# Performance work log

Hardware: AMD Instinct MI355X
Metric: run time of the kernel (lower is better)

## Reference

```python
import jax, jax.numpy as jnp
import numpy as np

N_NODES = 50000
N_EDGES = 600000
N_GRAPHS = 128
D = 128
L = 3
OUT = 10
BN_EPS = 1e-5


def setup_inputs() -> dict:
    key = jax.random.key(0)
    ks = jax.random.split(key, 8)
    x = jax.random.normal(ks[0], (N_NODES, D), dtype=jnp.float32)
    edge_index = jax.random.randint(ks[1], (2, N_EDGES), 0, N_NODES, dtype=jnp.int64)
    batch = jnp.sort(jax.random.randint(ks[2], (N_NODES,), 0, N_GRAPHS, dtype=jnp.int64))
    s = 0.05
    return {
        "x": x,
        "edge_index": edge_index,
        "batch": batch,
        "convW1": jax.random.normal(ks[3], (L, D, D), dtype=jnp.float32) * s,
        "convb1": jnp.zeros((L, D), dtype=jnp.float32),
        "convg": jnp.ones((L, D), dtype=jnp.float32),
        "convbt": jnp.zeros((L, D), dtype=jnp.float32),
        "convW2": jax.random.normal(ks[4], (L, D, D), dtype=jnp.float32) * s,
        "convb2": jnp.zeros((L, D), dtype=jnp.float32),
        "mW1": jax.random.normal(ks[5], (D, D), dtype=jnp.float32) * s,
        "mb1": jnp.zeros((D,), dtype=jnp.float32),
        "mg": jnp.ones((D,), dtype=jnp.float32),
        "mbt": jnp.zeros((D,), dtype=jnp.float32),
        "mW2": jax.random.normal(ks[6], (D, OUT), dtype=jnp.float32) * s,
        "mb2": jnp.zeros((OUT,), dtype=jnp.float32),
    }


def _mlp(h, W1, b1, g, bt, W2, b2):
    # PyG MLP: Linear -> BatchNorm(eval: mean=0, var=1) -> ReLU -> Linear (plain last)
    inv = 1.0 / jnp.sqrt(1.0 + BN_EPS)
    h = h @ W1 + b1
    h = jnp.maximum(h * (inv * g) + bt, 0.0)
    return h @ W2 + b2


def reference(x, edge_index, batch, convW1, convb1, convg, convbt, convW2, convb2,
              mW1, mb1, mg, mbt, mW2, mb2):
    src, dst = edge_index[0], edge_index[1]
    for l in range(L):
        # GINConv (eps=0): nn(x + scatter-add of neighbor features)
        agg = jax.ops.segment_sum(x[src], dst, num_segments=N_NODES)  # [N, D]
        x = _mlp(x + agg, convW1[l], convb1[l], convg[l], convbt[l], convW2[l], convb2[l])
        x = jnp.maximum(x, 0.0)  # .relu() after conv
    pooled = jax.ops.segment_sum(x, batch, num_segments=N_GRAPHS)  # [G, D]
    return _mlp(pooled, mW1, mb1, mg, mbt, mW2, mb2)  # [G, OUT]
```

## Files before the change

### kernel.cpp

```cpp
#include <hip/hip_runtime.h>

#define N_NODES 50000
#define N_EDGES 600000
#define N_GRAPHS 128
#define DIM 128
#define NLAYERS 3
#define NOUT 10
#define ELLW 48
#define LSTRIDE 136
#define ZROW N_NODES

typedef unsigned short u16;
typedef __attribute__((ext_vector_type(8))) short bf16x8;
typedef __attribute__((ext_vector_type(4))) float f32x4;

__device__ __forceinline__ float bf2f(u16 v) {
    unsigned u = ((unsigned)v) << 16;
    return __builtin_bit_cast(float, u);
}
__device__ __forceinline__ u16 f2bf(float f) {
    unsigned u = __builtin_bit_cast(unsigned, f);
    u = u + 0x7fffu + ((u >> 16) & 1u);
    return (u16)(u >> 16);
}

__global__ void zero_small(int* __restrict__ deg, float* __restrict__ pooled) {
    int i = blockIdx.x * blockDim.x + threadIdx.x;
    if (i < N_NODES) deg[i] = 0;
    if (i < N_GRAPHS * DIM) pooled[i] = 0.f;
}

__global__ void prep_all(int* __restrict__ deg, u16* __restrict__ ell,
                         const int* __restrict__ srcs, const int* __restrict__ dsts,
                         u16* __restrict__ xb, u16* __restrict__ bufA, u16* __restrict__ bufB,
                         const float* __restrict__ x, u16* __restrict__ Wswz,
                         const float* __restrict__ convW1, const float* __restrict__ convW2) {
    int i = blockIdx.x * blockDim.x + threadIdx.x;
    if (i < N_EDGES) {
        int d = dsts[i];
        int slot = atomicAdd(&deg[d], 1);
        if (slot < ELLW) ell[(size_t)d * ELLW + slot] = (u16)srcs[i];
    }
    if (i < DIM) {
        xb[(size_t)ZROW * DIM + i] = 0;
        bufA[(size_t)ZROW * DIM + i] = 0;
        bufB[(size_t)ZROW * DIM + i] = 0;
    }
    if (i < 6 * 16384) {
        int j = i & 7, lane = (i >> 3) & 63, cb = (i >> 9) & 7, kc = (i >> 12) & 3, w = i >> 14;
        int k = kc * 32 + ((lane >> 4) << 3) + j;
        int c = (cb << 4) + (lane & 15);
        const float* W = (w < 3) ? (convW1 + (size_t)w * 16384) : (convW2 + (size_t)(w - 3) * 16384);
        Wswz[i] = f2bf(W[k * DIM + c]);
    }
    if (i < N_NODES * DIM / 4) {
        float4 v = ((const float4*)x)[i];
        ushort4 o;
        o.x = f2bf(v.x); o.y = f2bf(v.y); o.z = f2bf(v.z); o.w = f2bf(v.w);
        ((ushort4*)xb)[i] = o;
    }
}

template <int POOL>
__global__ __launch_bounds__(256) void layer_fused(
    u16* __restrict__ out, const u16* __restrict__ x,
    const int* __restrict__ deg, const u16* __restrict__ ell,
    const u16* __restrict__ W1f, const u16* __restrict__ W2f,
    const float* __restrict__ b1, const float* __restrict__ g1,
    const float* __restrict__ bt1, const float* __restrict__ b2,
    const int* __restrict__ batch, float* __restrict__ pooled) {
    __shared__ u16 A[16 * LSTRIDE];
    __shared__ u16 H[16 * LSTRIDE];
    __shared__ int gb[16];
    const int tid = threadIdx.x;
    const int wv = tid >> 6;
    const int lane = tid & 63;
    const int row0 = blockIdx.x * 16;

    if (POOL && tid < 16) gb[tid] = batch[row0 + tid];

    const size_t coff = (size_t)lane * 2;
    {
        const int r0 = wv << 2;
        int len[4];
        const u16* ep[4];
        float ax[4], ay[4];
#pragma unroll
        for (int r = 0; r < 4; ++r) {
            const int grow = row0 + r0 + r;
            len[r] = min(deg[grow], ELLW);
            ep[r] = ell + (size_t)grow * ELLW;
            ushort2 self = *(const ushort2*)(x + (size_t)grow * DIM + coff);
            ax[r] = bf2f(self.x);
            ay[r] = bf2f(self.y);
        }
        const int maxlen = max(max(len[0], len[1]), max(len[2], len[3]));
        for (int j = 0; j < maxlen; j += 4) {
            int id[4][4];
#pragma unroll
            for (int r = 0; r < 4; ++r) {
                ushort4 e = *(const ushort4*)(ep[r] + j);
                id[r][0] = (j + 0 < len[r]) ? (int)e.x : ZROW;
                id[r][1] = (j + 1 < len[r]) ? (int)e.y : ZROW;
                id[r][2] = (j + 2 < len[r]) ? (int)e.z : ZROW;
                id[r][3] = (j + 3 < len[r]) ? (int)e.w : ZROW;
            }
#pragma unroll
            for (int r = 0; r < 4; ++r) {
                float px = 0.f, py = 0.f;
#pragma unroll
                for (int t = 0; t < 4; ++t) {
                    ushort2 v = *(const ushort2*)(x + (size_t)id[r][t] * DIM + coff);
                    px += bf2f(v.x);
                    py += bf2f(v.y);
                }
                ax[r] += px;
                ay[r] += py;
            }
        }
#pragma unroll
        for (int r = 0; r < 4; ++r) {
            ushort2 o;
            o.x = f2bf(ax[r]);
            o.y = f2bf(ay[r]);
            *(ushort2*)&A[(r0 + r) * LSTRIDE + lane * 2] = o;
        }
    }
    __syncthreads();

    const float inv = rsqrtf(1.f + 1e-5f);
    const int col0 = lane & 15;
    const int rbl = (lane >> 4) << 2;
    const int fragoff = (lane & 15) * LSTRIDE + ((lane >> 4) << 3);

    {
        f32x4 acc[2];
        acc[0] = (f32x4){0.f, 0.f, 0.f, 0.f};
        acc[1] = (f32x4){0.f, 0.f, 0.f, 0.f};
#pragma unroll
        for (int kc = 0; kc < 4; ++kc) {
            bf16x8 a = *(const bf16x8*)&A[fragoff + kc * 32];
#pragma unroll
            for (int m = 0; m < 2; ++m) {
                const int cb = (wv << 1) + m;
                bf16x8 bb = *(const bf16x8*)(W1f + ((((kc << 3) + cb) << 6 | lane) << 3));
                acc[m] = __builtin_amdgcn_mfma_f32_16x16x32_bf16(a, bb, acc[m], 0, 0, 0);
            }
        }
#pragma unroll
        for (int m = 0; m < 2; ++m) {
            const int c = (((wv << 1) + m) << 4) + col0;
            const float bias = b1[c];
            const float sg = inv * g1[c];
            const float st = bt1[c];
#pragma unroll
            for (int q = 0; q < 4; ++q) {
                float v = (acc[m][q] + bias) * sg + st;
                H[(rbl + q) * LSTRIDE + c] = f2bf(fmaxf(v, 0.f));
            }
        }
    }
    __syncthreads();

    {
        f32x4 acc[2];
        acc[0] = (f32x4){0.f, 0.f, 0.f, 0.f};
        acc[1] = (f32x4){0.f, 0.f, 0.f, 0.f};
#pragma unroll
        for (int kc = 0; kc < 4; ++kc) {
            bf16x8 a = *(const bf16x8*)&H[fragoff + kc * 32];
#pragma unroll
            for (int m = 0; m < 2; ++m) {
                const int cb = (wv << 1) + m;
                bf16x8 bb = *(const bf16x8*)(W2f + ((((kc << 3) + cb) << 6 | lane) << 3));
                acc[m] = __builtin_amdgcn_mfma_f32_16x16x32_bf16(a, bb, acc[m], 0, 0, 0);
            }
        }
#pragma unroll
        for (int m = 0; m < 2; ++m) {
            const int c = (((wv << 1) + m) << 4) + col0;
            const float bias = b2[c];
#pragma unroll
            for (int q = 0; q < 4; ++q) {
                float v = acc[m][q] + bias;
                A[(rbl + q) * LSTRIDE + c] = f2bf(fmaxf(v, 0.f));
            }
        }
    }
    __syncthreads();

    if (!POOL) {
        const int r = tid >> 4;
        const int seg = tid & 15;
        uint4 v = *(const uint4*)&A[r * LSTRIDE + seg * 8];
        *(uint4*)(out + (size_t)(row0 + r) * DIM + seg * 8) = v;
    } else {
        const int c = tid & 127;
        const int rbeg = (tid >> 7) << 3;
        float acc = 0.f;
        int curg = gb[rbeg];
#pragma unroll
        for (int r = 0; r < 8; ++r) {
            const int g = gb[rbeg + r];
            if (g != curg) {
                atomicAdd(&pooled[(size_t)curg * DIM + c], acc);
                acc = 0.f;
                curg = g;
            }
            acc += bf2f(A[(rbeg + r) * LSTRIDE + c]);
        }
        atomicAdd(&pooled[(size_t)curg * DIM + c], acc);
    }
}

__global__ __launch_bounds__(128) void tail_mlp(float* __restrict__ out,
                                                const float* __restrict__ pooled,
                                                const float* __restrict__ mW1,
                                                const float* __restrict__ mb1,
                                                const float* __restrict__ mg,
                                                const float* __restrict__ mbt,
                                                const float* __restrict__ mW2,
                                                const float* __restrict__ mb2) {
    const int g = blockIdx.x;
    const int c = threadIdx.x;
    __shared__ float pl[DIM];
    __shared__ float hd[DIM];
    pl[c] = pooled[(size_t)g * DIM + c];
    __syncthreads();

    float s = 0.f;
#pragma unroll 4
    for (int k = 0; k < DIM; ++k) s += pl[k] * mW1[k * DIM + c];
    const float inv = rsqrtf(1.f + 1e-5f);
    s = (s + mb1[c]) * (inv * mg[c]) + mbt[c];
    hd[c] = fmaxf(s, 0.f);
    __syncthreads();

    if (c < NOUT) {
        float o = 0.f;
#pragma unroll 4
        for (int k = 0; k < DIM; ++k) o += hd[k] * mW2[k * NOUT + c];
        out[g * NOUT + c] = o + mb2[c];
    }
}

extern "C" void kernel_launch(void* const* d_in, const int* in_sizes, int n_in,
                              void* d_out, int out_size, void* d_ws, size_t ws_size,
                              hipStream_t stream) {
    const float* x      = (const float*)d_in[0];
    const int*   ei     = (const int*)d_in[1];
    const int*   batch  = (const int*)d_in[2];
    const float* convW1 = (const float*)d_in[3];
    const float* convb1 = (const float*)d_in[4];
    const float* convg  = (const float*)d_in[5];
    const float* convbt = (const float*)d_in[6];
    const float* convW2 = (const float*)d_in[7];
    const float* convb2 = (const float*)d_in[8];
    const float* mW1    = (const float*)d_in[9];
    const float* mb1    = (const float*)d_in[10];
    const float* mg     = (const float*)d_in[11];
    const float* mbt    = (const float*)d_in[12];
    const float* mW2    = (const float*)d_in[13];
    const float* mb2    = (const float*)d_in[14];
    float* out = (float*)d_out;

    const int* srcs = ei;
    const int* dsts = ei + N_EDGES;

    const size_t NFP = (size_t)(N_NODES + 1) * DIM;
    u16* xb0  = (u16*)d_ws;
    u16* bufA = xb0 + NFP;
    u16* bufB = bufA + NFP;
    u16* Wswz = bufB + NFP;
    float* pooled = (float*)(Wswz + 6 * 16384);
    int* deg = (int*)(pooled + N_GRAPHS * DIM);
    u16* ell = (u16*)(deg + N_NODES);

    zero_small<<<(N_NODES + 255) / 256, 256, 0, stream>>>(deg, pooled);
    prep_all<<<(N_NODES * DIM / 4 + 255) / 256, 256, 0, stream>>>(
        deg, ell, srcs, dsts, xb0, bufA, bufB, x, Wswz, convW1, convW2);

    const int layerBlocks = N_NODES / 16;
    layer_fused<0><<<layerBlocks, 256, 0, stream>>>(
        bufA, xb0, deg, ell, Wswz, Wswz + (size_t)3 * 16384,
        convb1, convg, convbt, convb2, batch, pooled);
    layer_fused<0><<<layerBlocks, 256, 0, stream>>>(
        bufB, bufA, deg, ell, Wswz + (size_t)1 * 16384, Wswz + (size_t)4 * 16384,
        convb1 + DIM, convg + DIM, convbt + DIM, convb2 + DIM, batch, pooled);
    layer_fused<1><<<layerBlocks, 256, 0, stream>>>(
        bufA , bufB, deg, ell, Wswz + (size_t)2 * 16384, Wswz + (size_t)5 * 16384,
        convb1 + 2 * DIM, convg + 2 * DIM, convbt + 2 * DIM, convb2 + 2 * DIM, batch, pooled);

    tail_mlp<<<N_GRAPHS, 128, 0, stream>>>(out, pooled, mW1, mb1, mg, mbt, mW2, mb2);
}
```

Before: 154.8 us.

## Build ELL adjacency via two-pass bucketing with shared-memory per-bucket assembly

Replaces per-node global atomics and scattered 2-byte ELL writes with a two-phase build. Edges are first binned into 128-node buckets using one global atomic per edge on 391 counters. A new kernel then assembles each bucket's ELL rows in shared memory and writes them out with coalesced 16-byte stores. This adds a kernel launch and an intermediate buffer, and raises contention on the bucket counters. Edges beyond the bucket capacity of 2048 are silently dropped, which is only safe while the average is around 1536 per bucket.

```diff
diff --git a/kernel.cpp b/kernel.cpp
--- a/kernel.cpp
+++ b/kernel.cpp
@@ -9,8 +9,11 @@
 #define ELLW 48
 #define LSTRIDE 136
 #define ZROW N_NODES
+#define NBKT 391
+#define BKT_CAP 2048
 
 typedef unsigned short u16;
+typedef unsigned int u32;
 typedef __attribute__((ext_vector_type(8))) short bf16x8;
 typedef __attribute__((ext_vector_type(4))) float f32x4;
 
@@ -24,13 +27,13 @@
     return (u16)(u >> 16);
 }
 
-__global__ void zero_small(int* __restrict__ deg, float* __restrict__ pooled) {
+__global__ void zero_small(int* __restrict__ bcnt, float* __restrict__ pooled) {
     int i = blockIdx.x * blockDim.x + threadIdx.x;
-    if (i < N_NODES) deg[i] = 0;
+    if (i < NBKT) bcnt[i] = 0;
     if (i < N_GRAPHS * DIM) pooled[i] = 0.f;
 }
 
-__global__ void prep_all(int* __restrict__ deg, u16* __restrict__ ell,
+__global__ void prep_all(int* __restrict__ bcnt, u32* __restrict__ bpairs,
                          const int* __restrict__ srcs, const int* __restrict__ dsts,
                          u16* __restrict__ xb, u16* __restrict__ bufA, u16* __restrict__ bufB,
                          const float* __restrict__ x, u16* __restrict__ Wswz,
@@ -38,8 +41,10 @@
     int i = blockIdx.x * blockDim.x + threadIdx.x;
     if (i < N_EDGES) {
         int d = dsts[i];
-        int slot = atomicAdd(&deg[d], 1);
-        if (slot < ELLW) ell[(size_t)d * ELLW + slot] = (u16)srcs[i];
+        int b = d >> 7;
+        int pos = atomicAdd(&bcnt[b], 1);
+        if (pos < BKT_CAP)
+            bpairs[(size_t)b * BKT_CAP + pos] = ((u32)srcs[i] << 16) | (u32)(d & 127);
     }
     if (i < DIM) {
         xb[(size_t)ZROW * DIM + i] = 0;
@@ -58,6 +63,36 @@
         ushort4 o;
         o.x = f2bf(v.x); o.y = f2bf(v.y); o.z = f2bf(v.z); o.w = f2bf(v.w);
         ((ushort4*)xb)[i] = o;
+    }
+}
+
+__global__ __launch_bounds__(256) void ell_build(u16* __restrict__ ell, int* __restrict__ deg,
+                                                 const u32* __restrict__ bpairs,
+                                                 const int* __restrict__ bcnt) {
+    __shared__ u16 ell_s[128 * ELLW];
+    __shared__ int deg_s[128];
+    const int b = blockIdx.x;
+    const int tid = threadIdx.x;
+    if (tid < 128) deg_s[tid] = 0;
+    __syncthreads();
+
+    const int cnt = min(bcnt[b], BKT_CAP);
+    const u32* bp = bpairs + (size_t)b * BKT_CAP;
+    for (int i = tid; i < cnt; i += 256) {
+        u32 p = bp[i];
+        int local = (int)(p & 0xFFFFu);
+        int slot = atomicAdd(&deg_s[local], 1);
+        if (slot < ELLW) ell_s[local * ELLW + slot] = (u16)(p >> 16);
+    }
+    __syncthreads();
+
+    const int node0 = b << 7;
+    if (tid < 128 && node0 + tid < N_NODES) deg[node0 + tid] = deg_s[tid];
+    u16* eout = ell + (size_t)node0 * ELLW;
+#pragma unroll
+    for (int t = 0; t < 3; ++t) {
+        const int i = tid + t * 256;
+        *(uint4*)(eout + i * 8) = *(const uint4*)(ell_s + i * 8);
     }
 }
 
@@ -273,12 +308,15 @@
     u16* bufB = bufA + NFP;
     u16* Wswz = bufB + NFP;
     float* pooled = (float*)(Wswz + 6 * 16384);
-    int* deg = (int*)(pooled + N_GRAPHS * DIM);
-    u16* ell = (u16*)(deg + N_NODES);
-
-    zero_small<<<(N_NODES + 255) / 256, 256, 0, stream>>>(deg, pooled);
+    int* bcnt = (int*)(pooled + N_GRAPHS * DIM);
+    int* deg  = bcnt + 512;
+    u32* bpairs = (u32*)(deg + N_NODES);
+    u16* ell = (u16*)(bpairs + (size_t)NBKT * BKT_CAP);
+
+    zero_small<<<(N_GRAPHS * DIM + 255) / 256, 256, 0, stream>>>(bcnt, pooled);
     prep_all<<<(N_NODES * DIM / 4 + 255) / 256, 256, 0, stream>>>(
-        deg, ell, srcs, dsts, xb0, bufA, bufB, x, Wswz, convW1, convW2);
+        bcnt, bpairs, srcs, dsts, xb0, bufA, bufB, x, Wswz, convW1, convW2);
+    ell_build<<<NBKT, 256, 0, stream>>>(ell, deg, bpairs, bcnt);
 
     const int layerBlocks = N_NODES / 16;
     layer_fused<0><<<layerBlocks, 256, 0, stream>>>(
```

Result: slower. 336.9 us (+117.6%).

## Process 32 rows per block in fused GIN layer and split prep kernel

Applied to the files above, without the earlier changes.

Doubles the row tile of the fused layer kernel from 16 to 32 rows, so each wave gathers 8 rows and issues two MFMA row tiles per weight fragment load. This halves the per-row cost of loading weights and reduces the block count, but raises register pressure and the gather loop now runs to the maximum degree over 8 rows. Out-of-range rows are clamped to the zero row and their stores are masked. The prep kernel is also split into separate edge-to-ELL and conversion kernels.

```diff
diff --git a/kernel.cpp b/kernel.cpp
--- a/kernel.cpp
+++ b/kernel.cpp
@@ -9,8 +9,10 @@
 #define ELLW 48
 #define LSTRIDE 136
 #define ZROW N_NODES
+#define TROWS 32
 
 typedef unsigned short u16;
+typedef unsigned int u32;
 typedef __attribute__((ext_vector_type(8))) short bf16x8;
 typedef __attribute__((ext_vector_type(4))) float f32x4;
 
@@ -26,21 +28,23 @@
 
 __global__ void zero_small(int* __restrict__ deg, float* __restrict__ pooled) {
     int i = blockIdx.x * blockDim.x + threadIdx.x;
-    if (i < N_NODES) deg[i] = 0;
+    if (i < N_NODES + 16) deg[i] = 0;
     if (i < N_GRAPHS * DIM) pooled[i] = 0.f;
 }
 
-__global__ void prep_all(int* __restrict__ deg, u16* __restrict__ ell,
-                         const int* __restrict__ srcs, const int* __restrict__ dsts,
-                         u16* __restrict__ xb, u16* __restrict__ bufA, u16* __restrict__ bufB,
+__global__ void prep_ell(int* __restrict__ deg, u16* __restrict__ ell,
+                         const int* __restrict__ srcs, const int* __restrict__ dsts) {
+    int i = blockIdx.x * blockDim.x + threadIdx.x;
+    if (i >= N_EDGES) return;
+    int d = dsts[i];
+    int slot = atomicAdd(&deg[d], 1);
+    if (slot < ELLW) ell[(size_t)d * ELLW + slot] = (u16)srcs[i];
+}
+
+__global__ void prep_cvt(u16* __restrict__ xb, u16* __restrict__ bufA, u16* __restrict__ bufB,
                          const float* __restrict__ x, u16* __restrict__ Wswz,
                          const float* __restrict__ convW1, const float* __restrict__ convW2) {
     int i = blockIdx.x * blockDim.x + threadIdx.x;
-    if (i < N_EDGES) {
-        int d = dsts[i];
-        int slot = atomicAdd(&deg[d], 1);
-        if (slot < ELLW) ell[(size_t)d * ELLW + slot] = (u16)srcs[i];
-    }
     if (i < DIM) {
         xb[(size_t)ZROW * DIM + i] = 0;
         bufA[(size_t)ZROW * DIM + i] = 0;
@@ -69,36 +73,38 @@
     const float* __restrict__ b1, const float* __restrict__ g1,
     const float* __restrict__ bt1, const float* __restrict__ b2,
     const int* __restrict__ batch, float* __restrict__ pooled) {
-    __shared__ u16 A[16 * LSTRIDE];
-    __shared__ u16 H[16 * LSTRIDE];
-    __shared__ int gb[16];
+    __shared__ u16 A[TROWS * LSTRIDE];
+    __shared__ u16 H[TROWS * LSTRIDE];
+    __shared__ int gb[TROWS];
     const int tid = threadIdx.x;
     const int wv = tid >> 6;
     const int lane = tid & 63;
-    const int row0 = blockIdx.x * 16;
-
-    if (POOL && tid < 16) gb[tid] = batch[row0 + tid];
+    const int row0 = blockIdx.x * TROWS;
+
+    if (POOL && tid < TROWS) gb[tid] = batch[min(row0 + tid, N_NODES - 1)];
 
     const size_t coff = (size_t)lane * 2;
     {
-        const int r0 = wv << 2;
-        int len[4];
-        const u16* ep[4];
-        float ax[4], ay[4];
-#pragma unroll
-        for (int r = 0; r < 4; ++r) {
-            const int grow = row0 + r0 + r;
+        const int r0 = wv << 3;
+        int len[8];
+        const u16* ep[8];
+        float ax[8], ay[8];
+#pragma unroll
+        for (int r = 0; r < 8; ++r) {
+            const int grow = min(row0 + r0 + r, ZROW);
             len[r] = min(deg[grow], ELLW);
             ep[r] = ell + (size_t)grow * ELLW;
             ushort2 self = *(const ushort2*)(x + (size_t)grow * DIM + coff);
             ax[r] = bf2f(self.x);
             ay[r] = bf2f(self.y);
         }
-        const int maxlen = max(max(len[0], len[1]), max(len[2], len[3]));
+        int maxlen = 0;
+#pragma unroll
+        for (int r = 0; r < 8; ++r) maxlen = max(maxlen, len[r]);
         for (int j = 0; j < maxlen; j += 4) {
-            int id[4][4];
-#pragma unroll
-            for (int r = 0; r < 4; ++r) {
+            int id[8][4];
+#pragma unroll
+            for (int r = 0; r < 8; ++r) {
                 ushort4 e = *(const ushort4*)(ep[r] + j);
                 id[r][0] = (j + 0 < len[r]) ? (int)e.x : ZROW;
                 id[r][1] = (j + 1 < len[r]) ? (int)e.y : ZROW;
@@ -106,7 +112,7 @@
                 id[r][3] = (j + 3 < len[r]) ? (int)e.w : ZROW;
             }
 #pragma unroll
-            for (int r = 0; r < 4; ++r) {
+            for (int r = 0; r < 8; ++r) {
                 float px = 0.f, py = 0.f;
 #pragma unroll
                 for (int t = 0; t < 4; ++t) {
@@ -119,7 +125,7 @@
             }
         }
 #pragma unroll
-        for (int r = 0; r < 4; ++r) {
+        for (int r = 0; r < 8; ++r) {
             ushort2 o;
             o.x = f2bf(ax[r]);
             o.y = f2bf(ay[r]);
@@ -131,20 +137,25 @@
     const float inv = rsqrtf(1.f + 1e-5f);
     const int col0 = lane & 15;
     const int rbl = (lane >> 4) << 2;
-    const int fragoff = (lane & 15) * LSTRIDE + ((lane >> 4) << 3);
+    const int fo0 = (lane & 15) * LSTRIDE + ((lane >> 4) << 3);
+    const int fo1 = (16 + (lane & 15)) * LSTRIDE + ((lane >> 4) << 3);
 
     {
-        f32x4 acc[2];
-        acc[0] = (f32x4){0.f, 0.f, 0.f, 0.f};
-        acc[1] = (f32x4){0.f, 0.f, 0.f, 0.f};
+        f32x4 acc[2][2];
+#pragma unroll
+        for (int rt = 0; rt < 2; ++rt)
+#pragma unroll
+            for (int m = 0; m < 2; ++m) acc[rt][m] = (f32x4){0.f, 0.f, 0.f, 0.f};
 #pragma unroll
         for (int kc = 0; kc < 4; ++kc) {
-            bf16x8 a = *(const bf16x8*)&A[fragoff + kc * 32];
+            bf16x8 a0 = *(const bf16x8*)&A[fo0 + kc * 32];
+            bf16x8 a1 = *(const bf16x8*)&A[fo1 + kc * 32];
 #pragma unroll
             for (int m = 0; m < 2; ++m) {
                 const int cb = (wv << 1) + m;
                 bf16x8 bb = *(const bf16x8*)(W1f + ((((kc << 3) + cb) << 6 | lane) << 3));
-                acc[m] = __builtin_amdgcn_mfma_f32_16x16x32_bf16(a, bb, acc[m], 0, 0, 0);
+                acc[0][m] = __builtin_amdgcn_mfma_f32_16x16x32_bf16(a0, bb, acc[0][m], 0, 0, 0);
+                acc[1][m] = __builtin_amdgcn_mfma_f32_16x16x32_bf16(a1, bb, acc[1][m], 0, 0, 0);
             }
         }
 #pragma unroll
@@ -154,26 +165,33 @@
             const float sg = inv * g1[c];
             const float st = bt1[c];
 #pragma unroll
-            for (int q = 0; q < 4; ++q) {
-                float v = (acc[m][q] + bias) * sg + st;
-                H[(rbl + q) * LSTRIDE + c] = f2bf(fmaxf(v, 0.f));
+            for (int rt = 0; rt < 2; ++rt) {
+#pragma unroll
+                for (int q = 0; q < 4; ++q) {
+                    float v = (acc[rt][m][q] + bias) * sg + st;
+                    H[(rt * 16 + rbl + q) * LSTRIDE + c] = f2bf(fmaxf(v, 0.f));
+                }
             }
         }
     }
     __syncthreads();
 
     {
-        f32x4 acc[2];
-        acc[0] = (f32x4){0.f, 0.f, 0.f, 0.f};
-        acc[1] = (f32x4){0.f, 0.f, 0.f, 0.f};
+        f32x4 acc[2][2];
+#pragma unroll
+        for (int rt = 0; rt < 2; ++rt)
+#pragma unroll
+            for (int m = 0; m < 2; ++m) acc[rt][m] = (f32x4){0.f, 0.f, 0.f, 0.f};
 #pragma unroll
         for (int kc = 0; kc < 4; ++kc) {
-            bf16x8 a = *(const bf16x8*)&H[fragoff + kc * 32];
+            bf16x8 a0 = *(const bf16x8*)&H[fo0 + kc * 32];
+            bf16x8 a1 = *(const bf16x8*)&H[fo1 + kc * 32];
 #pragma unroll
             for (int m = 0; m < 2; ++m) {
                 const int cb = (wv << 1) + m;
                 bf16x8 bb = *(const bf16x8*)(W2f + ((((kc << 3) + cb) << 6 | lane) << 3));
-                acc[m] = __builtin_amdgcn_mfma_f32_16x16x32_bf16(a, bb, acc[m], 0, 0, 0);
+                acc[0][m] = __builtin_amdgcn_mfma_f32_16x16x32_bf16(a0, bb, acc[0][m], 0, 0, 0);
+                acc[1][m] = __builtin_amdgcn_mfma_f32_16x16x32_bf16(a1, bb, acc[1][m], 0, 0, 0);
             }
         }
 #pragma unroll
@@ -181,26 +199,33 @@
             const int c = (((wv << 1) + m) << 4) + col0;
             const float bias = b2[c];
 #pragma unroll
-            for (int q = 0; q < 4; ++q) {
-                float v = acc[m][q] + bias;
-                A[(rbl + q) * LSTRIDE + c] = f2bf(fmaxf(v, 0.f));
+            for (int rt = 0; rt < 2; ++rt) {
+#pragma unroll
+                for (int q = 0; q < 4; ++q) {
+                    float v = acc[rt][m][q] + bias;
+                    A[(rt * 16 + rbl + q) * LSTRIDE + c] = f2bf(fmaxf(v, 0.f));
+                }
             }
         }
     }
     __syncthreads();
 
     if (!POOL) {
-        const int r = tid >> 4;
-        const int seg = tid & 15;
-        uint4 v = *(const uint4*)&A[r * LSTRIDE + seg * 8];
-        *(uint4*)(out + (size_t)(row0 + r) * DIM + seg * 8) = v;
+#pragma unroll
+        for (int it = 0; it < 2; ++it) {
+            const int r = (tid >> 4) + it * 16;
+            const int seg = tid & 15;
+            const int grow = row0 + r;
+            uint4 v = *(const uint4*)&A[r * LSTRIDE + seg * 8];
+            if (grow < N_NODES) *(uint4*)(out + (size_t)grow * DIM + seg * 8) = v;
+        }
     } else {
         const int c = tid & 127;
-        const int rbeg = (tid >> 7) << 3;
+        const int rbeg = (tid >> 7) << 4;
         float acc = 0.f;
         int curg = gb[rbeg];
 #pragma unroll
-        for (int r = 0; r < 8; ++r) {
+        for (int r = 0; r < 16; ++r) {
             const int g = gb[rbeg + r];
             if (g != curg) {
                 atomicAdd(&pooled[(size_t)curg * DIM + c], acc);
@@ -274,13 +299,14 @@
     u16* Wswz = bufB + NFP;
     float* pooled = (float*)(Wswz + 6 * 16384);
     int* deg = (int*)(pooled + N_GRAPHS * DIM);
-    u16* ell = (u16*)(deg + N_NODES);
-
-    zero_small<<<(N_NODES + 255) / 256, 256, 0, stream>>>(deg, pooled);
-    prep_all<<<(N_NODES * DIM / 4 + 255) / 256, 256, 0, stream>>>(
-        deg, ell, srcs, dsts, xb0, bufA, bufB, x, Wswz, convW1, convW2);
-
-    const int layerBlocks = N_NODES / 16;
+    u16* ell = (u16*)(deg + N_NODES + 16);
+
+    zero_small<<<(N_NODES + 16 + 255) / 256, 256, 0, stream>>>(deg, pooled);
+    prep_ell<<<(N_EDGES + 255) / 256, 256, 0, stream>>>(deg, ell, srcs, dsts);
+    prep_cvt<<<(N_NODES * DIM / 4 + 255) / 256, 256, 0, stream>>>(
+        xb0, bufA, bufB, x, Wswz, convW1, convW2);
+
+    const int layerBlocks = (N_NODES + TROWS - 1) / TROWS;
     layer_fused<0><<<layerBlocks, 256, 0, stream>>>(
         bufA, xb0, deg, ell, Wswz, Wswz + (size_t)3 * 16384,
         convb1, convg, convbt, convb2, batch, pooled);
```

New measurement: 187.7 us. 1.21x slower.
